# Kernel tuning notes

Hardware: AMD Instinct MI355X
Metric: run time of the kernel (lower is better)

The kernel has to match this reference:

```python
import jax, jax.numpy as jnp
import numpy as np
from jax.scipy.special import logsumexp

NTRANS = 40          # 2 * nbase * (nbase + 1) with nbase = 4
NBASE = 4
# cat-mod index groups: A:[can, 6mA_1, 6mA_2], C:[can, 5mC], G:[can], T:[can, modT]
CAN_INDICES = [np.array([0, 1, 2]), np.array([0, 3]), np.array([0]), np.array([0, 4])]


def global_norm_flipflop(scores):
    """scores: [T, N, 40] -> globally normalized scores [T, N, 40]."""
    T, N, C = scores.shape
    nbase = NBASE
    two_nb = 2 * nbase
    # fwd = zeros, then normalized: logZ0 = log(2*nbase)
    logZ0 = jnp.full((N, 1), jnp.log(float(two_nb)), scores.dtype)
    fwd0 = jnp.full((N, two_nb), -jnp.log(float(two_nb)), scores.dtype)

    def step(carry, scores_t):
        fwd, logZ = carry
        # [N, nbase+1, 2*nbase]
        curr = fwd[:, None, :] + scores_t.reshape(N, nbase + 1, two_nb)
        base1 = logsumexp(curr[:, :nbase, :], axis=2)                 # [N, nbase]
        base2 = jnp.logaddexp(curr[:, nbase, :nbase], curr[:, nbase, nbase:])  # [N, nbase]
        new_state = jnp.concatenate([base1, base2], axis=1)           # [N, 2*nbase]
        factors = logsumexp(new_state, axis=1, keepdims=True)         # [N, 1]
        new_state = new_state - factors
        return (new_state, logZ + factors), None

    (fwd, logZ), _ = jax.lax.scan(step, (fwd0, logZ0), scores)
    return scores - logZ[None, :, :] / T


def setup_inputs() -> dict:
    key = jax.random.key(0)
    k1, k2, k3 = jax.random.split(key, 3)
    T, N, D, S = 2000, 256, 256, 45
    x = jax.random.normal(k1, (T, N, D), dtype=jnp.float32)
    W = jax.random.normal(k2, (S, D), dtype=jnp.float32) * (1.0 / np.sqrt(D))
    b = jax.random.normal(k3, (S,), dtype=jnp.float32) * 0.5
    return {"x": x, "W": W, "b": b}


def reference(x, W, b):
    # Linear: [T, N, D] @ [D, S] + b
    y = jnp.einsum("tnd,sd->tns", x, W) + b
    trans_scores = 5.0 * jnp.tanh(y[:, :, :NTRANS])
    cat_mod_scores = y[:, :, NTRANS:]                 # [T, N, nmod+1] = [T, N, 5]
    norm_trans = global_norm_flipflop(trans_scores)   # [T, N, 40]
    mod_layers = [jax.nn.log_softmax(cat_mod_scores[:, :, idx], axis=2)
                  for idx in CAN_INDICES]
    cat_mods = jnp.concatenate(mod_layers, axis=2)    # [T, N, 8]
    return jnp.concatenate([norm_trans, cat_mods], axis=2)  # [T, N, 48]
```

## Files before the change

### kernel.cpp

```cpp
#include <hip/hip_runtime.h>
#include <hip/hip_bf16.h>
#include <math.h>

#define TT 2000
#define NN 256
#define DD 256
#define SS 45
#define SOUT 48
#define NTRANS_C 40
#define CHUNKS 40
#define CLEN 50
#define BK 32
#define NCH (DD / BK)
#define XPAD 40

typedef __attribute__((ext_vector_type(8))) short bf16x8;
typedef __attribute__((ext_vector_type(4))) float f32x4;

__device__ inline ushort f2bf_rne(float f) {
    unsigned u = __float_as_uint(f);
    unsigned r = u + 0x7fffu + ((u >> 16) & 1u);
    return (ushort)(r >> 16);
}
__device__ __forceinline__ int cvtpk(float lo, float hi) {
    int r;
    asm("v_cvt_pk_bf16_f32 %0, %1, %2" : "=v"(r) : "v"(lo), "v"(hi));
    return r;
}
__device__ __host__ __forceinline__ constexpr int sidx(int c) {
    return (c < 32) ? (4 * (c & 7) + (c >> 3))
         : (c < 36) ? (32 + 2 * (c - 32))
         : (c < 40) ? (32 + 2 * (c - 36) + 1)
         : c;
}
__device__ __forceinline__ int swz_idx(int s, int koff) {
    return s * DD + ((((koff >> 3) ^ (s & 7)) << 3) | (koff & 7));
}

__global__ __launch_bounds__(256) void kPrep(const float* __restrict__ W,
                                             const float* __restrict__ b,
                                             ushort* __restrict__ Whi,
                                             float* __restrict__ b48) {
    const int s = blockIdx.x;
    const int k = threadIdx.x;
    const float wv = (s < SS) ? W[s * DD + k] : 0.f;
    Whi[s * DD + k] = f2bf_rne(wv);
    if (k == 0) b48[s] = (s < SS) ? b[s] : 0.f;
}

__global__ __launch_bounds__(512, 6) void kA_mfma(const float* __restrict__ x,
                                                  const ushort* __restrict__ Whi,
                                                  const float* __restrict__ b48,
                                                  ushort* __restrict__ sc) {
    __shared__ ushort Wl[SOUT * DD];
    __shared__ ushort xw[8][16 * XPAD];
    const int tid = threadIdx.x;
    for (int idx = tid; idx < SOUT * (DD / 8); idx += 512) {
        const int s = idx >> 5;
        const int c8 = (idx & 31) * 8;
        const uint4 v = *reinterpret_cast<const uint4*>(Whi + s * DD + c8);
        *reinterpret_cast<uint4*>(&Wl[swz_idx(s, c8)]) = v;
    }
    __syncthreads();

    const int l = tid & 63, w = tid >> 6;
    const long m0 = (long)blockIdx.x * 128;
    const int r16 = l & 15;
    const int kg = l >> 4;
    const int lrow = l >> 3;
    const int lcol = (l & 7) * 4;
    const float* xp = x + (m0 + w * 16 + lrow) * DD + lcol;
    const float* xq = xp + 8 * DD;
    ushort* xs = xw[w];
    int2* xw0 = reinterpret_cast<int2*>(&xs[lrow * XPAD + lcol]);
    int2* xw1 = reinterpret_cast<int2*>(&xs[(lrow + 8) * XPAD + lcol]);
    const bf16x8* xrd = reinterpret_cast<const bf16x8*>(&xs[r16 * XPAD + kg * 8]);

    f32x4 acc[3] = {{0, 0, 0, 0}, {0, 0, 0, 0}, {0, 0, 0, 0}};

    float4 pf[2][2];
    pf[0][0] = *reinterpret_cast<const float4*>(xp + 0);
    pf[0][1] = *reinterpret_cast<const float4*>(xq + 0);
    pf[1][0] = *reinterpret_cast<const float4*>(xp + BK);
    pf[1][1] = *reinterpret_cast<const float4*>(xq + BK);

#pragma unroll
    for (int c = 0; c < NCH; ++c) {
        const float4 pa = pf[c & 1][0];
        const float4 qa = pf[c & 1][1];
        xw0->x = cvtpk(pa.x, pa.y);
        xw0->y = cvtpk(pa.z, pa.w);
        xw1->x = cvtpk(qa.x, qa.y);
        xw1->y = cvtpk(qa.z, qa.w);
        if (c + 2 < NCH) {
            pf[c & 1][0] = *reinterpret_cast<const float4*>(xp + (c + 2) * BK);
            pf[c & 1][1] = *reinterpret_cast<const float4*>(xq + (c + 2) * BK);
        }
        __builtin_amdgcn_sched_barrier(0);
        const bf16x8 a = *xrd;
        const int koff = c * BK + kg * 8;
        const bf16x8 b0 = *reinterpret_cast<const bf16x8*>(&Wl[swz_idx(0 * 16 + r16, koff)]);
        const bf16x8 b1 = *reinterpret_cast<const bf16x8*>(&Wl[swz_idx(1 * 16 + r16, koff)]);
        const bf16x8 b2 = *reinterpret_cast<const bf16x8*>(&Wl[swz_idx(2 * 16 + r16, koff)]);
        acc[0] = __builtin_amdgcn_mfma_f32_16x16x32_bf16(a, b0, acc[0], 0, 0, 0);
        acc[1] = __builtin_amdgcn_mfma_f32_16x16x32_bf16(a, b1, acc[1], 0, 0, 0);
        acc[2] = __builtin_amdgcn_mfma_f32_16x16x32_bf16(a, b2, acc[2], 0, 0, 0);
    }

    __syncthreads();
    ushort* se = Wl;
#pragma unroll
    for (int jt = 0; jt < 3; ++jt) {
        const int col = jt * 16 + r16;
        const float bias = b48[col];
        int si;
        if (jt < 2) si = 4 * (col & 7) + (col >> 3);
        else if (r16 < 8) si = (r16 < 4) ? (32 + 2 * r16) : (32 + 2 * (r16 - 4) + 1);
        else si = 40 + (r16 - 8);
#pragma unroll
        for (int r = 0; r < 4; ++r) {
            const int lr = w * 16 + kg * 4 + r;
            const float y = acc[jt][r] + bias;
            float v;
            if (col < NTRANS_C) {
                const float e = __expf(2.f * y);
                v = 5.f * (1.f - 2.f / (e + 1.f));
            } else {
                v = y;
            }
            se[lr * SOUT + si] = f2bf_rne(v);
        }
    }
    __syncthreads();
    const uint4* su = reinterpret_cast<const uint4*>(se);
    uint4* du = reinterpret_cast<uint4*>(sc + m0 * SOUT);
    du[tid] = su[tid];
    if (tid < 256) du[512 + tid] = su[512 + tid];
}

#define DPP_XOR1 0xB1
#define DPP_XOR2 0x4E

__device__ inline float fmax_x1(float v) {
    const int d = __builtin_amdgcn_mov_dpp(__float_as_int(v), DPP_XOR1, 0xF, 0xF, true);
    return fmaxf(v, __int_as_float(d));
}
__device__ inline float fmax_x2(float v) {
    const int d = __builtin_amdgcn_mov_dpp(__float_as_int(v), DPP_XOR2, 0xF, 0xF, true);
    return fmaxf(v, __int_as_float(d));
}
__device__ inline float add_x1(float v) {
    const int d = __builtin_amdgcn_mov_dpp(__float_as_int(v), DPP_XOR1, 0xF, 0xF, true);
    return v + __int_as_float(d);
}
__device__ inline float add_x2(float v) {
    const int d = __builtin_amdgcn_mov_dpp(__float_as_int(v), DPP_XOR2, 0xF, 0xF, true);
    return v + __int_as_float(d);
}
__device__ inline float swz4(float v) {
    return __int_as_float(__builtin_amdgcn_ds_swizzle(__float_as_int(v), 0x101F));
}
__device__ inline float fmax_x4(float v) { return fmaxf(v, swz4(v)); }
__device__ inline float add_x4(float v) { return v + swz4(v); }
__device__ inline float sum8(float v) { return add_x4(add_x2(add_x1(v))); }
__device__ inline float max8(float v) { return fmax_x4(fmax_x2(fmax_x1(v))); }
__device__ inline float gat_k(float v) {
    return __int_as_float(__builtin_amdgcn_ds_swizzle(__float_as_int(v), 0x001B));
}
__device__ __forceinline__ float bperm(int byteaddr, float v) {
    return __int_as_float(__builtin_amdgcn_ds_bpermute(byteaddr, __float_as_int(v)));
}

__global__ __launch_bounds__(64) void kB_scan(const ushort* __restrict__ sc,
                                              float* __restrict__ gbuf) {
    const int n = blockIdx.x;
    const int c = blockIdx.y;
    const int l = threadIdx.x;
    const int col = l >> 3;
    const int j = l & 7;
    const int k = j & 3;
    const int ls = (l < 40) ? sidx(l) : 0;
    const int a0 = 4 * j, a1 = 4 * (8 + j), a2 = 4 * (16 + j), a3 = 4 * (24 + j);
    const int aa = 4 * (32 + k), ab = 4 * (36 + k);

    float P = (j == col) ? 1.f : 0.f;
    int scale = 0;
    const long stride = (long)NN * SOUT;
    const ushort* sp = sc + ((long)(c * CLEN) * NN + n) * SOUT;

    float Eo = __expf(__uint_as_float(((unsigned)sp[ls]) << 16));
    float e0 = bperm(a0, Eo), e1 = bperm(a1, Eo), e2 = bperm(a2, Eo),
          e3 = bperm(a3, Eo), ea = bperm(aa, Eo), eb = bperm(ab, Eo);

    for (int t = 0; t < CLEN; ++t) {
        const ushort* np = sp + stride;
        const ushort nxt = (t + 1 < CLEN) ? np[ls] : (ushort)0;
        float p0 = sum8(P * e0);
        float p1 = sum8(P * e1);
        float p2 = sum8(P * e2);
        float p3 = sum8(P * e3);
        const float pb = fmaf(gat_k(P), ea, P * eb);
        const float pl = (j < 2) ? ((j == 0) ? p0 : p1)
                                 : ((j == 2) ? p2 : p3);
        P = (j < 4) ? pl : pb;
        if ((t & 3) == 3) {
            const float Mx = max8(P);
            const int ex = ((__float_as_int(Mx) >> 23) & 255) - 127;
            P *= __int_as_float((unsigned)(127 - ex) << 23);
            scale += ex;
        }
        Eo = __expf(__uint_as_float(((unsigned)nxt) << 16));
        e0 = bperm(a0, Eo); e1 = bperm(a1, Eo); e2 = bperm(a2, Eo);
        e3 = bperm(a3, Eo); ea = bperm(aa, Eo); eb = bperm(ab, Eo);
        sp = np;
    }
    const float m = __logf(P) + (float)scale * 0.6931471805599453f;
    gbuf[((long)(n * CHUNKS + c)) * 64 + l] = m;
}

__device__ inline float lse8(float v) {
    const float m = max8(v);
    return m + __logf(sum8(__expf(v - m)));
}
__device__ inline float lse64(float v) {
    float m = v;
#pragma unroll
    for (int d = 1; d < 64; d <<= 1) m = fmaxf(m, __shfl_xor(m, d));
    float e = __expf(v - m);
#pragma unroll
    for (int d = 1; d < 64; d <<= 1) e += __shfl_xor(e, d);
    return m + __logf(e);
}

__global__ __launch_bounds__(64) void kC_combine(const float* __restrict__ gbuf,
                                                 float* __restrict__ logZT) {
    const int n = blockIdx.x;
    const int l = threadIdx.x;
    const int gi = (l & 7) * 8 + (l >> 3);
    float g[CHUNKS];
#pragma unroll
    for (int c = 0; c < CHUNKS; ++c)
        g[c] = gbuf[((long)(n * CHUNKS + c)) * 64 + gi];
    float u = -logf(8.f);
#pragma unroll
    for (int c = 0; c < CHUNKS; ++c) {
        const float nu = lse8(g[c] + u);
        u = __shfl(nu, ((l & 7) << 3) | (l >> 3));
    }
    const float z = lse64(u);
    if (l == 0) logZT[n] = z / (float)TT;
}

__global__ __launch_bounds__(128) void kD_final(const ushort* __restrict__ sc,
                                                const float* __restrict__ logZT,
                                                float* __restrict__ out) {
    __shared__ float dout[128 * SOUT];
    const int tid = threadIdx.x;
    const long row0 = (long)blockIdx.x * 128;
    const long row = row0 + tid;
    const int n = (int)(row & (NN - 1));
    const float z = logZT[n];
    const ushort* srow = sc + row * SOUT;
    float st[48];
#pragma unroll
    for (int i = 0; i < 6; ++i) {
        const uint4 q = reinterpret_cast<const uint4*>(srow)[i];
        const unsigned wv[4] = {q.x, q.y, q.z, q.w};
#pragma unroll
        for (int t = 0; t < 4; ++t) {
            st[8 * i + 2 * t]     = __uint_as_float(wv[t] << 16);
            st[8 * i + 2 * t + 1] = __uint_as_float(wv[t] & 0xffff0000u);
        }
    }
    float* a = &dout[tid * SOUT];
#pragma unroll
    for (int c = 0; c < 40; ++c) a[c] = st[sidx(c)] - z;
    const float y40 = st[40], y41 = st[41], y42 = st[42], y43 = st[43], y44 = st[44];
    const float m3 = fmaxf(fmaxf(y40, y41), y42);
    const float l3 = m3 + __logf(__expf(y40 - m3) + __expf(y41 - m3) + __expf(y42 - m3));
    a[40] = y40 - l3; a[41] = y41 - l3; a[42] = y42 - l3;
    const float mA = fmaxf(y40, y43);
    const float lA = mA + __logf(__expf(y40 - mA) + __expf(y43 - mA));
    a[43] = y40 - lA; a[44] = y43 - lA;
    a[45] = 0.f;
    const float mB = fmaxf(y40, y44);
    const float lB = mB + __logf(__expf(y40 - mB) + __expf(y44 - mB));
    a[46] = y40 - lB; a[47] = y44 - lB;
    __syncthreads();
    const float4* sf = reinterpret_cast<const float4*>(dout);
    float4* df = reinterpret_cast<float4*>(out + row0 * SOUT);
#pragma unroll
    for (int kq = 0; kq < 12; ++kq)
        df[kq * 128 + tid] = sf[kq * 128 + tid];
}

extern "C" void kernel_launch(void* const* d_in, const int* in_sizes, int n_in,
                              void* d_out, int out_size, void* d_ws, size_t ws_size,
                              hipStream_t stream) {
    const float* x = (const float*)d_in[0];
    const float* W = (const float*)d_in[1];
    const float* b = (const float*)d_in[2];
    float* out = (float*)d_out;

    ushort* sc   = (ushort*)d_ws;
    float* gbuf  = (float*)((char*)d_ws + 49152000);
    float* logZT = gbuf + (long)NN * CHUNKS * 64;
    float* b48   = logZT + NN;
    ushort* Whi  = (ushort*)(b48 + SOUT);

    hipLaunchKernelGGL(kPrep, dim3(SOUT), dim3(DD), 0, stream, W, b, Whi, b48);
    hipLaunchKernelGGL(kA_mfma, dim3((TT * NN) / 128), dim3(512), 0, stream, x, Whi, b48, sc);
    hipLaunchKernelGGL(kB_scan, dim3(NN, CHUNKS), dim3(64), 0, stream, sc, gbuf);
    hipLaunchKernelGGL(kC_combine, dim3(NN), dim3(64), 0, stream, gbuf, logZT);
    hipLaunchKernelGGL(kD_final, dim3((TT * NN) / 128), dim3(128), 0, stream, sc, logZT, out);
}
```

Measured before the change: 206.3 us.

## Restructure chunk scan: two chunks per wave, LDS-staged exp scores

```diff
diff --git a/kernel.cpp b/kernel.cpp
--- a/kernel.cpp
+++ b/kernel.cpp
@@ -164,58 +164,76 @@
 __device__ inline float add_x4(float v) { return v + swz4(v); }
 __device__ inline float sum8(float v) { return add_x4(add_x2(add_x1(v))); }
 __device__ inline float max8(float v) { return fmax_x4(fmax_x2(fmax_x1(v))); }
-__device__ inline float gat_k(float v) {
-    return __int_as_float(__builtin_amdgcn_ds_swizzle(__float_as_int(v), 0x001B));
-}
-__device__ __forceinline__ float bperm(int byteaddr, float v) {
-    return __int_as_float(__builtin_amdgcn_ds_bpermute(byteaddr, __float_as_int(v)));
-}
 
 __global__ __launch_bounds__(64) void kB_scan(const ushort* __restrict__ sc,
                                               float* __restrict__ gbuf) {
+    __shared__ float el[2][2][48];
     const int n = blockIdx.x;
-    const int c = blockIdx.y;
     const int l = threadIdx.x;
-    const int col = l >> 3;
-    const int j = l & 7;
-    const int k = j & 3;
-    const int ls = (l < 40) ? sidx(l) : 0;
-    const int a0 = 4 * j, a1 = 4 * (8 + j), a2 = 4 * (16 + j), a3 = 4 * (24 + j);
-    const int aa = 4 * (32 + k), ab = 4 * (36 + k);
-
-    float P = (j == col) ? 1.f : 0.f;
+    const int h = l >> 5;
+    const int l32 = l & 31;
+    const int d = l32 & 3;
+    const int q = l32 >> 2;
+    const int ch = blockIdx.y * 2 + h;
+    const long stride = (long)NN * SOUT;
+    const ushort* sp = sc + ((long)(ch * CLEN) * NN + n) * SOUT;
+
+    float Plo = (d == q) ? 1.f : 0.f;
+    float Phi = (4 + d == q) ? 1.f : 0.f;
     int scale = 0;
-    const long stride = (long)NN * SOUT;
-    const ushort* sp = sc + ((long)(c * CLEN) * NN + n) * SOUT;
-
-    float Eo = __expf(__uint_as_float(((unsigned)sp[ls]) << 16));
-    float e0 = bperm(a0, Eo), e1 = bperm(a1, Eo), e2 = bperm(a2, Eo),
-          e3 = bperm(a3, Eo), ea = bperm(aa, Eo), eb = bperm(ab, Eo);
+    float* eh = &el[h][0][0];
+
+    {
+        const float s1 = __uint_as_float(((unsigned)sp[l32]) << 16);
+        eh[l32] = __expf(s1);
+        if (l32 < 8) {
+            const float s2 = __uint_as_float(((unsigned)sp[32 + l32]) << 16);
+            eh[32 + l32] = __expf(s2);
+        }
+    }
 
     for (int t = 0; t < CLEN; ++t) {
-        const ushort* np = sp + stride;
-        const ushort nxt = (t + 1 < CLEN) ? np[ls] : (ushort)0;
-        float p0 = sum8(P * e0);
-        float p1 = sum8(P * e1);
-        float p2 = sum8(P * e2);
-        float p3 = sum8(P * e3);
-        const float pb = fmaf(gat_k(P), ea, P * eb);
-        const float pl = (j < 2) ? ((j == 0) ? p0 : p1)
-                                 : ((j == 2) ? p2 : p3);
-        P = (j < 4) ? pl : pb;
+        const float* er = eh + (t & 1) * 48;
+        const float4 Elo = *reinterpret_cast<const float4*>(er + 4 * d);
+        const float4 Ehi = *reinterpret_cast<const float4*>(er + 16 + 4 * d);
+        const float2 Eab = *reinterpret_cast<const float2*>(er + 32 + 2 * d);
+        if (t + 1 < CLEN) {
+            const ushort* np = sp + stride;
+            float* ew = eh + ((t + 1) & 1) * 48;
+            const float s1 = __uint_as_float(((unsigned)np[l32]) << 16);
+            ew[l32] = __expf(s1);
+            if (l32 < 8) {
+                const float s2 = __uint_as_float(((unsigned)np[32 + l32]) << 16);
+                ew[32 + l32] = __expf(s2);
+            }
+            sp = np;
+        }
+        float v0 = fmaf(Plo, Elo.x, Phi * Ehi.x);
+        float v1 = fmaf(Plo, Elo.y, Phi * Ehi.y);
+        float v2 = fmaf(Plo, Elo.z, Phi * Ehi.z);
+        float v3 = fmaf(Plo, Elo.w, Phi * Ehi.w);
+        v0 = add_x2(add_x1(v0));
+        v1 = add_x2(add_x1(v1));
+        v2 = add_x2(add_x1(v2));
+        v3 = add_x2(add_x1(v3));
+        const float PhiN = fmaf(Plo, Eab.x, Phi * Eab.y);
+        const float pa_ = (d & 1) ? v1 : v0;
+        const float pb_ = (d & 1) ? v3 : v2;
+        Plo = (d & 2) ? pb_ : pa_;
+        Phi = PhiN;
         if ((t & 3) == 3) {
-            const float Mx = max8(P);
+            const float Mx = fmax_x2(fmax_x1(fmaxf(Plo, Phi)));
             const int ex = ((__float_as_int(Mx) >> 23) & 255) - 127;
-            P *= __int_as_float((unsigned)(127 - ex) << 23);
+            const float s = __int_as_float((unsigned)(127 - ex) << 23);
+            Plo *= s;
+            Phi *= s;
             scale += ex;
         }
-        Eo = __expf(__uint_as_float(((unsigned)nxt) << 16));
-        e0 = bperm(a0, Eo); e1 = bperm(a1, Eo); e2 = bperm(a2, Eo);
-        e3 = bperm(a3, Eo); ea = bperm(aa, Eo); eb = bperm(ab, Eo);
-        sp = np;
-    }
-    const float m = __logf(P) + (float)scale * 0.6931471805599453f;
-    gbuf[((long)(n * CHUNKS + c)) * 64 + l] = m;
+    }
+    const float base = (float)scale * 0.6931471805599453f;
+    float* gb = gbuf + ((long)(n * CHUNKS + ch)) * 64;
+    gb[q * 8 + d] = __logf(Plo) + base;
+    gb[q * 8 + 4 + d] = __logf(Phi) + base;
 }
 
 __device__ inline float lse8(float v) {
@@ -264,8 +282,8 @@
     float st[48];
 #pragma unroll
     for (int i = 0; i < 6; ++i) {
-        const uint4 q = reinterpret_cast<const uint4*>(srow)[i];
-        const unsigned wv[4] = {q.x, q.y, q.z, q.w};
+        const uint4 qv = reinterpret_cast<const uint4*>(srow)[i];
+        const unsigned wv[4] = {qv.x, qv.y, qv.z, qv.w};
 #pragma unroll
         for (int t = 0; t < 4; ++t) {
             st[8 * i + 2 * t]     = __uint_as_float(wv[t] << 16);
@@ -310,7 +328,7 @@
 
     hipLaunchKernelGGL(kPrep, dim3(SOUT), dim3(DD), 0, stream, W, b, Whi, b48);
     hipLaunchKernelGGL(kA_mfma, dim3((TT * NN) / 128), dim3(512), 0, stream, x, Whi, b48, sc);
-    hipLaunchKernelGGL(kB_scan, dim3(NN, CHUNKS), dim3(64), 0, stream, sc, gbuf);
+    hipLaunchKernelGGL(kB_scan, dim3(NN, CHUNKS / 2), dim3(64), 0, stream, sc, gbuf);
     hipLaunchKernelGGL(kC_combine, dim3(NN), dim3(64), 0, stream, gbuf, logZT);
     hipLaunchKernelGGL(kD_final, dim3((TT * NN) / 128), dim3(128), 0, stream, sc, logZT, out);
 }
```

New measurement: 195.7 us. 1.05x faster.
